# Optimization experiments

Hardware: AMD Instinct MI355X
Metric: run time of the kernel (lower is better)

The kernel has to match this reference:

```python
import jax, jax.numpy as jnp
import numpy as np

B = 16384; HB = 120; BD = 9; NS = 32; NF = 15  # history_bars, bar_descr, n_skills, n_forecast


def _lin_attn(x, wq, wk, wv, wo, bo, g, b):
    # x: [N, S, D_in]; linear attention with phi = elu + 1, residual + LayerNorm
    phi = lambda z: jax.nn.elu(z) + 1.0
    Q = phi(jnp.einsum('nsd,ed->nse', x, wq))
    K = phi(jnp.einsum('nsd,ed->nse', x, wk))
    V = jnp.einsum('nsd,ed->nse', x, wv)
    kv = jnp.einsum('nsd,nse->nde', K, V)              # [N, D, D]
    num = jnp.einsum('nsd,nde->nse', Q, kv)
    den = jnp.maximum(jnp.sum(Q * jnp.sum(K, axis=1, keepdims=True), axis=-1, keepdims=True), 1e-6)
    o = num / den
    y = jnp.einsum('nse,fe->nsf', o, wo) + bo + o      # out_proj + residual
    mu = jnp.mean(y, axis=-1, keepdims=True)
    var = jnp.var(y, axis=-1, keepdims=True)
    return (y - mu) * jax.lax.rsqrt(var + 1e-5) * g + b


def _forward(x, bn_g, bn_b, bn_m, bn_v, wq2, wk2, wv2, wo2, bo2, ln2g, ln2b,
             wq4, wk4, wv4, wo4, bo4, ln4g, ln4b,
             w_ih, w_hh, b_ih, b_hh, cg_w, cg_uw, cg_ub,
             w6, b6, w7, b7, rev_w, rev_b):
    Bn = x.shape[0]
    # BatchNorm1d (eval mode, running stats)
    out = (x - bn_m) * jax.lax.rsqrt(bn_v + 1e-5) * bn_g + bn_b
    # lin_attn_2: tokens = 120 time steps, d = 9 variables
    out = _lin_attn(out.reshape(Bn, HB, BD), wq2, wk2, wv2, wo2, bo2, ln2g, ln2b)
    # transpose_3: [B, 120, 9] -> [B, 9, 120]
    out = jnp.transpose(out, (0, 2, 1))
    # lin_attn_4: 9 parallel sequences of one 120-dim token
    out = _lin_attn(out.reshape(Bn * BD, 1, HB), wq4, wk4, wv4, wo4, bo4, ln4g, ln4b)
    # CGLSTM over 120 steps, vectorized across (batch * 9 variables)
    xs = jnp.transpose(out.reshape(Bn * BD, HB, 1), (1, 0, 2))  # [120, B*9, 1]
    h0 = jnp.zeros((Bn * BD, NS), x.dtype)

    def step(carry, x_t):
        h, c = carry
        gates = x_t @ w_ih.T + b_ih + h @ w_hh.T + b_hh  # [N, 4*NS]
        i, f, g, o = jnp.split(gates, 4, axis=-1)         # torch LSTMCell gate order
        c_new = jax.nn.sigmoid(f) * c + jax.nn.sigmoid(i) * jnp.tanh(g)
        gc = jax.nn.sigmoid(x_t @ cg_w.T + h @ cg_uw.T + cg_ub)  # contextual gate uses old h
        h_new = gc * jnp.tanh(c_new)                      # LSTM's own h output is discarded
        return (h_new, c_new), None

    (h, _), _ = jax.lax.scan(step, (h0, h0), xs)
    cglstm_out = h.reshape(Bn, BD * NS)                   # [B, 288]
    # conv_6 (pointwise per variable) + softplus, conv_7 + tanh
    t = jax.nn.softplus(h @ w6.T + b6)                    # [B*9, 60]
    t = jnp.tanh(t @ w7.T + b7).reshape(Bn, NF * BD)      # [B, 135]
    # transpose_8: view [B,15,9] -> [B,9,15]
    y = jnp.transpose(t.reshape(Bn, NF, BD), (0, 2, 1)).reshape(Bn, -1)
    # RevIN (normalize over full 135-dim vector, unbiased std as in torch.std)
    mu = jnp.mean(y, axis=-1, keepdims=True)
    sd = jnp.maximum(jnp.std(y, axis=-1, keepdims=True, ddof=1), 1e-5)
    enc = (y - mu) / sd * rev_w + rev_b
    return cglstm_out, enc


def setup_inputs() -> dict:
    key = jax.random.key(0)
    ks = jax.random.split(key, 20)
    r = lambda i, s, sc=0.1: jax.random.normal(ks[i], s, jnp.float32) * sc
    return dict(
        x=jax.random.normal(ks[0], (B, HB * BD), jnp.float32),
        bn_g=jnp.ones((HB * BD,), jnp.float32), bn_b=jnp.zeros((HB * BD,), jnp.float32),
        bn_m=r(1, (HB * BD,)),
        bn_v=jax.random.uniform(ks[2], (HB * BD,), jnp.float32, 0.5, 1.5),
        wq2=r(3, (BD, BD), 0.3), wk2=r(4, (BD, BD), 0.3), wv2=r(5, (BD, BD), 0.3),
        wo2=r(6, (BD, BD), 0.3), bo2=jnp.zeros((BD,), jnp.float32),
        ln2g=jnp.ones((BD,), jnp.float32), ln2b=jnp.zeros((BD,), jnp.float32),
        wq4=r(7, (HB, HB), 0.05), wk4=r(8, (HB, HB), 0.05), wv4=r(9, (HB, HB), 0.05),
        wo4=r(10, (HB, HB), 0.05), bo4=jnp.zeros((HB,), jnp.float32),
        ln4g=jnp.ones((HB,), jnp.float32), ln4b=jnp.zeros((HB,), jnp.float32),
        w_ih=r(11, (4 * NS, 1), 0.2), w_hh=r(12, (4 * NS, NS), 0.1),
        b_ih=jnp.zeros((4 * NS,), jnp.float32), b_hh=jnp.zeros((4 * NS,), jnp.float32),
        cg_w=r(13, (NS, 1), 0.2), cg_uw=r(14, (NS, NS), 0.1), cg_ub=jnp.zeros((NS,), jnp.float32),
        w6=r(15, (4 * NF, NS), 0.15), b6=jnp.zeros((4 * NF,), jnp.float32),
        w7=r(16, (NF, 4 * NF), 0.15), b7=jnp.zeros((NF,), jnp.float32),
        rev_w=jnp.ones((BD * NF,), jnp.float32), rev_b=jnp.zeros((BD * NF,), jnp.float32),
    )


def reference(x, bn_g, bn_b, bn_m, bn_v, wq2, wk2, wv2, wo2, bo2, ln2g, ln2b,
              wq4, wk4, wv4, wo4, bo4, ln4g, ln4b,
              w_ih, w_hh, b_ih, b_hh, cg_w, cg_uw, cg_ub,
              w6, b6, w7, b7, rev_w, rev_b):
    return _forward(x, bn_g, bn_b, bn_m, bn_v, wq2, wk2, wv2, wo2, bo2, ln2g, ln2b,
                    wq4, wk4, wv4, wo4, bo4, ln4g, ln4b,
                    w_ih, w_hh, b_ih, b_hh, cg_w, cg_uw, cg_ub,
                    w6, b6, w7, b7, rev_w, rev_b)
```

## Files before the change

kernel.cpp:

```cpp
#include <hip/hip_runtime.h>
#include <math.h>

#define NTH 256
#define SB 7

typedef __attribute__((ext_vector_type(8))) short bf16x8;
typedef __attribute__((ext_vector_type(4))) float f32x4;

__device__ __forceinline__ float fast_sigmoid(float x) {
    return __builtin_amdgcn_rcpf(1.0f + __expf(-x));
}
__device__ __forceinline__ float fast_tanh(float x) {
    return fmaf(-2.0f, __builtin_amdgcn_rcpf(__expf(2.0f * x) + 1.0f), 1.0f);
}
__device__ __forceinline__ short f2bf(float x) {
    unsigned u = __float_as_uint(x);
    return (short)((u + 0x7FFFu + ((u >> 16) & 1u)) >> 16);
}

extern "C" __global__ void __launch_bounds__(NTH, 3)
se_kernel(const float* __restrict__ x,
          const float* __restrict__ bn_g, const float* __restrict__ bn_b,
          const float* __restrict__ bn_m, const float* __restrict__ bn_v,
          const float* __restrict__ wq2, const float* __restrict__ wk2,
          const float* __restrict__ wv2, const float* __restrict__ wo2,
          const float* __restrict__ bo2, const float* __restrict__ ln2g,
          const float* __restrict__ ln2b,
          const float* __restrict__ wq4, const float* __restrict__ wk4,
          const float* __restrict__ wv4, const float* __restrict__ wo4,
          const float* __restrict__ bo4, const float* __restrict__ ln4g,
          const float* __restrict__ ln4b,
          const float* __restrict__ w_ih, const float* __restrict__ w_hh,
          const float* __restrict__ b_ih, const float* __restrict__ b_hh,
          const float* __restrict__ cg_w, const float* __restrict__ cg_uw,
          const float* __restrict__ cg_ub,
          const float* __restrict__ w6, const float* __restrict__ b6,
          const float* __restrict__ w7, const float* __restrict__ b7,
          const float* __restrict__ rev_w, const float* __restrict__ rev_b,
          float* __restrict__ out, int Bn)
{
    __shared__ __align__(16) float sm[13552];
    const int tid  = threadIdx.x;
    const int lane = tid & 63;
    const int wv   = tid >> 6;
    const int b0   = blockIdx.x * SB;
    const int nsamp = min(SB, Bn - b0);

    float* sU  = sm;
    float* SCR = sm + 7560;
    float* sWQ2 = sm + 13192; float* sWK2 = sm + 13273;
    float* sWV2 = sm + 13354; float* sWO2 = sm + 13435;
    float* sBO2 = sm + 13516; float* sLN2G = sm + 13525; float* sLN2B = sm + 13534;
    float* sKV = sm + 11880;  float* sKS = sm + 11961;
    float* sBO4 = sm + 13192; float* sLN4G = sm + 13312; float* sLN4B = sm + 13432;
    float* sMU = sm + 11880;  float* sRS = sm + 11900;
    float* sST = sm + 11920;
    float* sH0 = SCR;
    float* sH1 = SCR + 2816;
    float* sT1 = sU;
    float* sTF = sU + 3780;

    for (int i = tid; i < 81; i += NTH) {
        sWQ2[i] = wq2[i]; sWK2[i] = wk2[i]; sWV2[i] = wv2[i]; sWO2[i] = wo2[i];
    }
    if (tid < 9) { sBO2[tid] = bo2[tid]; sLN2G[tid] = ln2g[tid]; sLN2B[tid] = ln2b[tid]; }
    __syncthreads();

    float* S0 = SCR; float* S1 = SCR + 1080; float* S2 = SCR + 2160; float* S3 = SCR + 3240;
    for (int ss = 0; ss < SB; ++ss) {
        if (ss < nsamp) {
            const int b = b0 + ss;
            for (int i = tid; i < 1080; i += NTH) {
                float xv = x[(size_t)b * 1080 + i];
                S0[i] = (xv - bn_m[i]) * rsqrtf(bn_v[i] + 1e-5f) * bn_g[i] + bn_b[i];
            }
            __syncthreads();
            for (int idx = tid; idx < 1080; idx += NTH) {
                int s = idx / 9, e = idx - s * 9;
                float aq = 0.f, ak = 0.f, av = 0.f;
                #pragma unroll
                for (int d = 0; d < 9; ++d) {
                    float xv = S0[s * 9 + d];
                    aq = fmaf(xv, sWQ2[e * 9 + d], aq);
                    ak = fmaf(xv, sWK2[e * 9 + d], ak);
                    av = fmaf(xv, sWV2[e * 9 + d], av);
                }
                S1[idx] = aq >= 0.f ? aq + 1.f : __expf(aq);
                S2[idx] = ak >= 0.f ? ak + 1.f : __expf(ak);
                S3[idx] = av;
            }
            __syncthreads();
            if (tid < 81) {
                int d = tid / 9, e = tid - d * 9;
                float acc = 0.f;
                for (int s = 0; s < 120; ++s) acc = fmaf(S2[s * 9 + d], S3[s * 9 + e], acc);
                sKV[tid] = acc;
            } else if (tid < 90) {
                int d = tid - 81;
                float acc = 0.f;
                for (int s = 0; s < 120; ++s) acc += S2[s * 9 + d];
                sKS[d] = acc;
            }
            __syncthreads();
            for (int idx = tid; idx < 1080; idx += NTH) {
                int s = idx / 9, e = idx - s * 9;
                float num = 0.f, den = 0.f;
                #pragma unroll
                for (int d = 0; d < 9; ++d) {
                    float qv = S1[s * 9 + d];
                    num = fmaf(qv, sKV[d * 9 + e], num);
                    den = fmaf(qv, sKS[d], den);
                }
                S0[idx] = num / fmaxf(den, 1e-6f);
            }
            __syncthreads();
            for (int idx = tid; idx < 1080; idx += NTH) {
                int s = idx / 9, f = idx - s * 9;
                float acc = sBO2[f] + S0[s * 9 + f];
                #pragma unroll
                for (int e = 0; e < 9; ++e) acc = fmaf(S0[s * 9 + e], sWO2[f * 9 + e], acc);
                S1[idx] = acc;
            }
            __syncthreads();
            if (tid < 120) {
                int s = tid;
                float sum = 0.f, sq = 0.f;
                #pragma unroll
                for (int f = 0; f < 9; ++f) { float v = S1[s * 9 + f]; sum += v; sq = fmaf(v, v, sq); }
                float mu = sum * (1.f / 9.f);
                float rs = rsqrtf(sq * (1.f / 9.f) - mu * mu + 1e-5f);
                #pragma unroll
                for (int f = 0; f < 9; ++f)
                    sU[(ss * 9 + f) * 120 + s] = (S1[s * 9 + f] - mu) * rs * sLN2G[f] + sLN2B[f];
            }
        }
        __syncthreads();
    }

    for (int i = tid; i < 120; i += NTH) { sBO4[i] = bo4[i]; sLN4G[i] = ln4g[i]; sLN4B[i] = ln4b[i]; }
    for (int p = 0; p < 4; ++p) {
        float* V0 = SCR;
        float* Y0 = SCR + 2160;
        const int sp = tid / 120, erow = tid - sp * 120;
        const int smp = p * 2 + sp;
        const bool act = (tid < 240) && (smp < SB);
        if (act) {
            const float* uB = sU + smp * 1080;
            float acc[9];
            #pragma unroll
            for (int v = 0; v < 9; ++v) acc[v] = 0.f;
            const float* w0p = &wv4[erow * 120];
            for (int dq = 0; dq < 30; ++dq) {
                float4 wA = *(const float4*)&w0p[dq * 4];
                #pragma unroll
                for (int v = 0; v < 9; ++v) {
                    float4 u = *(const float4*)&uB[v * 120 + dq * 4];
                    acc[v] = fmaf(wA.x, u.x, acc[v]); acc[v] = fmaf(wA.y, u.y, acc[v]);
                    acc[v] = fmaf(wA.z, u.z, acc[v]); acc[v] = fmaf(wA.w, u.w, acc[v]);
                }
            }
            float* dst = V0 + sp * 1080;
            #pragma unroll
            for (int v = 0; v < 9; ++v) dst[v * 120 + erow] = acc[v];
        }
        __syncthreads();
        if (act) {
            const float* vB = V0 + sp * 1080;
            float acc[9];
            #pragma unroll
            for (int v = 0; v < 9; ++v) acc[v] = 0.f;
            const float* w0p = &wo4[erow * 120];
            for (int dq = 0; dq < 30; ++dq) {
                float4 wA = *(const float4*)&w0p[dq * 4];
                #pragma unroll
                for (int v = 0; v < 9; ++v) {
                    float4 u = *(const float4*)&vB[v * 120 + dq * 4];
                    acc[v] = fmaf(wA.x, u.x, acc[v]); acc[v] = fmaf(wA.y, u.y, acc[v]);
                    acc[v] = fmaf(wA.z, u.z, acc[v]); acc[v] = fmaf(wA.w, u.w, acc[v]);
                }
            }
            float* Y = Y0 + sp * 1080;
            #pragma unroll
            for (int v = 0; v < 9; ++v)
                Y[v * 120 + erow] = acc[v] + sBO4[erow] + vB[v * 120 + erow];
        }
        __syncthreads();
        if (tid < 18 && (p * 2 + tid / 9) < SB) {
            int sp2 = tid / 9, v = tid - sp2 * 9;
            const float* Y = Y0 + sp2 * 1080 + v * 120;
            float sum = 0.f, sq = 0.f;
            for (int e = 0; e < 120; ++e) { float t = Y[e]; sum += t; sq = fmaf(t, t, sq); }
            float mu = sum * (1.f / 120.f);
            sMU[tid] = mu;
            sRS[tid] = rsqrtf(sq * (1.f / 120.f) - mu * mu + 1e-5f);
        }
        __syncthreads();
        for (int idx = tid; idx < 540; idx += NTH) {
            int sp2 = idx / 270, off = idx - sp2 * 270;
            int smp2 = p * 2 + sp2;
            int v = off / 30, qq = off - v * 30;
            if (smp2 < SB) {
                const float* Y = Y0 + sp2 * 1080;
                float4 y = *(const float4*)&Y[v * 120 + qq * 4];
                float4 g = *(const float4*)&sLN4G[qq * 4];
                float4 bb = *(const float4*)&sLN4B[qq * 4];
                float mu = sMU[sp2 * 9 + v], rs = sRS[sp2 * 9 + v];
                float4 o;
                o.x = (y.x - mu) * rs * g.x + bb.x;
                o.y = (y.y - mu) * rs * g.y + bb.y;
                o.z = (y.z - mu) * rs * g.z + bb.z;
                o.w = (y.w - mu) * rs * g.w + bb.w;
                *(float4*)&sU[(smp2 * 9 + v) * 120 + qq * 4] = o;
            }
        }
        __syncthreads();
    }

    for (int i = tid; i < 2816; i += NTH) sH0[i] = 0.f;
    __syncthreads();

    const int c = lane & 15, q = lane >> 4;
    bf16x8 bfr[8]; float wxv[8], bsv[8];
    int grow[4]; int pcol;
    {
        bf16x8 pa, pb, pa2, pb2;
        #pragma unroll
        for (int j = 0; j < 8; ++j) { pa[j] = 0; pb[j] = 0; pa2[j] = 0; pb2[j] = 0; }
        if (q == 0) {
            pa[0]  = f2bf((float)c); pb[0]  = f2bf(1.0f);
            pa2[0] = f2bf(1.0f);     pb2[0] = f2bf((float)c);
        }
        f32x4 zc; zc[0] = zc[1] = zc[2] = zc[3] = 0.f;
        f32x4 prr = __builtin_amdgcn_mfma_f32_16x16x32_bf16(pa,  pb,  zc, 0, 0, 0);
        f32x4 pcc = __builtin_amdgcn_mfma_f32_16x16x32_bf16(pa2, pb2, zc, 0, 0, 0);
        #pragma unroll
        for (int r = 0; r < 4; ++r) grow[r] = wv * 16 + (int)(prr[r] + 0.5f);
        pcol = (int)(pcc[0] + 0.5f);

        #pragma unroll
        for (int T = 0; T < 8; ++T) {
            int gate = T >> 1, kk = ((T & 1) << 4) + pcol;
            const float* wr; float wx, bs;
            if (gate < 3) {
                int n = gate * 32 + kk;
                wr = &w_hh[n * 32]; wx = w_ih[n]; bs = b_ih[n] + b_hh[n];
            } else {
                wr = &cg_uw[kk * 32]; wx = cg_w[kk]; bs = cg_ub[kk];
            }
            bf16x8 tv;
            #pragma unroll
            for (int j = 0; j < 8; ++j) tv[j] = f2bf(wr[q * 8 + j]);
            bfr[T] = tv; wxv[T] = wx; bsv[T] = bs;
        }
    }
    float cst[8];
    #pragma unroll
    for (int i = 0; i < 8; ++i) cst[i] = 0.f;
    const int live9 = nsamp * 9;
    const float* ar0 = &sH0[(wv * 16 + c) * 44 + q * 8];
    const float* ar1 = &sH1[(wv * 16 + c) * 44 + q * 8];

#define LSTM_STEP(RP, WPL, XARR)                                               \
    {                                                                          \
        float4 hA = *(const float4*)(RP);                                      \
        float4 hB = *(const float4*)((RP) + 4);                                \
        bf16x8 af;                                                             \
        af[0] = f2bf(hA.x); af[1] = f2bf(hA.y);                                \
        af[2] = f2bf(hA.z); af[3] = f2bf(hA.w);                                \
        af[4] = f2bf(hB.x); af[5] = f2bf(hB.y);                                \
        af[6] = f2bf(hB.z); af[7] = f2bf(hB.w);                                \
        f32x4 acc[8];                                                          \
        _Pragma("unroll")                                                      \
        for (int T = 0; T < 8; ++T) {                                          \
            f32x4 ci;                                                          \
            _Pragma("unroll")                                                  \
            for (int r = 0; r < 4; ++r) ci[r] = fmaf(wxv[T], XARR[r], bsv[T]); \
            acc[T] = __builtin_amdgcn_mfma_f32_16x16x32_bf16(af, bfr[T], ci, 0, 0, 0); \
        }                                                                      \
        _Pragma("unroll")                                                      \
        for (int kh = 0; kh < 2; ++kh) {                                       \
            _Pragma("unroll")                                                  \
            for (int r = 0; r < 4; ++r) {                                      \
                float si  = fast_sigmoid(acc[kh][r]);                          \
                float sf  = fast_sigmoid(acc[2 + kh][r]);                      \
                float tg  = fast_tanh(acc[4 + kh][r]);                         \
                float sgc = fast_sigmoid(acc[6 + kh][r]);                      \
                float cn = fmaf(sf, cst[kh * 4 + r], si * tg);                 \
                cst[kh * 4 + r] = cn;                                          \
                (WPL)[grow[r] * 44 + (kh << 4) + pcol] = sgc * fast_tanh(cn);  \
            }                                                                  \
        }                                                                      \
    }

    for (int t = 0; t < 120; t += 2) {
        float xa[4], xb[4];
        #pragma unroll
        for (int r = 0; r < 4; ++r) {
            float2 xv;
            if (grow[r] < live9) xv = *(const float2*)&sU[grow[r] * 120 + t];
            else { xv.x = 0.f; xv.y = 0.f; }
            xa[r] = xv.x; xb[r] = xv.y;
        }
        LSTM_STEP(ar0, sH1, xa)
        LSTM_STEP(ar1, sH0, xb)
    }
    __syncthreads();

    for (int idx = tid; idx < SB * 288; idx += NTH) {
        int ssd = idx / 288, r = idx - ssd * 288;
        if (ssd < nsamp) {
            int v = r >> 5, k = r & 31;
            out[(size_t)(b0 + ssd) * 288 + r] = sH0[(ssd * 9 + v) * 44 + k];
        }
    }

    for (int idx = tid; idx < SB * 540; idx += NTH) {
        int ssd = idx / 540, rem = idx - ssd * 540;
        int v = rem / 60, j = rem - v * 60;
        if (ssd < nsamp) {
            float acc = b6[j];
            const float4* wr4 = (const float4*)&w6[j * 32];
            const float4* hv = (const float4*)&sH0[(ssd * 9 + v) * 44];
            #pragma unroll
            for (int qq = 0; qq < 8; ++qq) {
                float4 w = wr4[qq], h = hv[qq];
                acc = fmaf(w.x, h.x, acc); acc = fmaf(w.y, h.y, acc);
                acc = fmaf(w.z, h.z, acc); acc = fmaf(w.w, h.w, acc);
            }
            sT1[idx] = acc > 15.f ? acc : log1pf(__expf(acc));
        }
    }
    __syncthreads();
    for (int idx = tid; idx < SB * 135; idx += NTH) {
        int ssd = idx / 135, rem = idx - ssd * 135;
        int v = rem / 15, f = rem - v * 15;
        if (ssd < nsamp) {
            float acc = b7[f];
            const float4* wr = (const float4*)&w7[f * 60];
            const float4* tv = (const float4*)&sT1[ssd * 540 + v * 60];
            #pragma unroll
            for (int qq = 0; qq < 15; ++qq) {
                float4 w = wr[qq], h = tv[qq];
                acc = fmaf(w.x, h.x, acc); acc = fmaf(w.y, h.y, acc);
                acc = fmaf(w.z, h.z, acc); acc = fmaf(w.w, h.w, acc);
            }
            sTF[idx] = fast_tanh(acc);
        }
    }
    __syncthreads();
    if (tid < SB && tid < nsamp) {
        const float* tf = &sTF[tid * 135];
        float sum = 0.f;
        for (int i = 0; i < 135; ++i) sum += tf[i];
        float mu = sum * (1.f / 135.f);
        float sq = 0.f;
        for (int i = 0; i < 135; ++i) { float d = tf[i] - mu; sq = fmaf(d, d, sq); }
        float sd = sqrtf(sq * (1.f / 134.f));
        sST[tid * 2]     = mu;
        sST[tid * 2 + 1] = 1.f / fmaxf(sd, 1e-5f);
    }
    __syncthreads();
    const size_t encbase = (size_t)Bn * 288;
    for (int idx = tid; idx < SB * 135; idx += NTH) {
        int ssd = idx / 135, j = idx - ssd * 135;
        if (ssd < nsamp) {
            int qq = j / 15, pp = j - qq * 15;
            float val = (sTF[ssd * 135 + pp * 9 + qq] - sST[ssd * 2]) * sST[ssd * 2 + 1] * rev_w[j] + rev_b[j];
            out[encbase + (size_t)(b0 + ssd) * 135 + j] = val;
        }
    }
}

extern "C" void kernel_launch(void* const* d_in, const int* in_sizes, int n_in,
                              void* d_out, int out_size, void* d_ws, size_t ws_size,
                              hipStream_t stream) {
    const float* x    = (const float*)d_in[0];
    const float* bn_g = (const float*)d_in[1];
    const float* bn_b = (const float*)d_in[2];
    const float* bn_m = (const float*)d_in[3];
    const float* bn_v = (const float*)d_in[4];
    const float* wq2  = (const float*)d_in[5];
    const float* wk2  = (const float*)d_in[6];
    const float* wv2  = (const float*)d_in[7];
    const float* wo2  = (const float*)d_in[8];
    const float* bo2  = (const float*)d_in[9];
    const float* ln2g = (const float*)d_in[10];
    const float* ln2b = (const float*)d_in[11];
    const float* wq4  = (const float*)d_in[12];
    const float* wk4  = (const float*)d_in[13];
    const float* wv4  = (const float*)d_in[14];
    const float* wo4  = (const float*)d_in[15];
    const float* bo4  = (const float*)d_in[16];
    const float* ln4g = (const float*)d_in[17];
    const float* ln4b = (const float*)d_in[18];
    const float* w_ih = (const float*)d_in[19];
    const float* w_hh = (const float*)d_in[20];
    const float* b_ih = (const float*)d_in[21];
    const float* b_hh = (const float*)d_in[22];
    const float* cg_w = (const float*)d_in[23];
    const float* cg_uw= (const float*)d_in[24];
    const float* cg_ub= (const float*)d_in[25];
    const float* w6   = (const float*)d_in[26];
    const float* b6   = (const float*)d_in[27];
    const float* w7   = (const float*)d_in[28];
    const float* b7   = (const float*)d_in[29];
    const float* rev_w= (const float*)d_in[30];
    const float* rev_b= (const float*)d_in[31];

    int Bn = in_sizes[0] / 1080;
    int grid = (Bn + SB - 1) / SB;
    hipLaunchKernelGGL(se_kernel, dim3(grid), dim3(NTH), 0, stream,
                       x, bn_g, bn_b, bn_m, bn_v, wq2, wk2, wv2, wo2, bo2, ln2g, ln2b,
                       wq4, wk4, wv4, wo4, bo4, ln4g, ln4b,
                       w_ih, w_hh, b_ih, b_hh, cg_w, cg_uw, cg_ub,
                       w6, b6, w7, b7, rev_w, rev_b,
                       (float*)d_out, Bn);
}
```

Baseline: 1.524 ms.

## Store intermediate activations in bf16 shared memory and use packed bf16 conversion

Stores the per-sample activation buffer sU as bf16 instead of fp32. This halves its shared-memory footprint and shrinks the LDS allocation from about 54KB to about 39KB, so more blocks may fit per CU. It also swaps the manual float-to-bf16 rounding in the LSTM step for the hardware v_cvt_pk_bf16_f32 instruction. The cost is lower precision for inputs to the attention projection and the LSTM, plus extra unpack shifts on every read.

```diff
diff --git a/kernel.cpp b/kernel.cpp
--- a/kernel.cpp
+++ b/kernel.cpp
@@ -6,6 +6,8 @@
 
 typedef __attribute__((ext_vector_type(8))) short bf16x8;
 typedef __attribute__((ext_vector_type(4))) float f32x4;
+typedef __attribute__((ext_vector_type(2))) unsigned short us2;
+typedef __attribute__((ext_vector_type(4))) unsigned short us4;
 
 __device__ __forceinline__ float fast_sigmoid(float x) {
     return __builtin_amdgcn_rcpf(1.0f + __expf(-x));
@@ -16,6 +18,14 @@
 __device__ __forceinline__ short f2bf(float x) {
     unsigned u = __float_as_uint(x);
     return (short)((u + 0x7FFFu + ((u >> 16) & 1u)) >> 16);
+}
+__device__ __forceinline__ unsigned pk_bf16(float lo, float hi) {
+    unsigned r;
+    asm("v_cvt_pk_bf16_f32 %0, %1, %2" : "=v"(r) : "v"(lo), "v"(hi));
+    return r;
+}
+__device__ __forceinline__ float bf2f(unsigned short u) {
+    return __uint_as_float(((unsigned)u) << 16);
 }
 
 extern "C" __global__ void __launch_bounds__(NTH, 3)
@@ -39,26 +49,26 @@
           const float* __restrict__ rev_w, const float* __restrict__ rev_b,
           float* __restrict__ out, int Bn)
 {
-    __shared__ __align__(16) float sm[13552];
+    __shared__ __align__(16) float sm[9862];
     const int tid  = threadIdx.x;
     const int lane = tid & 63;
     const int wv   = tid >> 6;
     const int b0   = blockIdx.x * SB;
     const int nsamp = min(SB, Bn - b0);
 
-    float* sU  = sm;
-    float* SCR = sm + 7560;
-    float* sWQ2 = sm + 13192; float* sWK2 = sm + 13273;
-    float* sWV2 = sm + 13354; float* sWO2 = sm + 13435;
-    float* sBO2 = sm + 13516; float* sLN2G = sm + 13525; float* sLN2B = sm + 13534;
-    float* sKV = sm + 11880;  float* sKS = sm + 11961;
-    float* sBO4 = sm + 13192; float* sLN4G = sm + 13312; float* sLN4B = sm + 13432;
-    float* sMU = sm + 11880;  float* sRS = sm + 11900;
-    float* sST = sm + 11920;
+    unsigned short* sUb = (unsigned short*)sm;
+    float* SCR = sm + 3780;
+    float* sKV = sm + 9412; float* sKS = sm + 9493;
+    float* sMU = sm + 9412; float* sRS = sm + 9430;
+    float* sST = sm + 9448;
+    float* sWQ2 = sm + 9502; float* sWK2 = sm + 9583;
+    float* sWV2 = sm + 9664; float* sWO2 = sm + 9745;
+    float* sBO2 = sm + 9826; float* sLN2G = sm + 9835; float* sLN2B = sm + 9844;
+    float* sBO4 = sm + 9502; float* sLN4G = sm + 9622; float* sLN4B = sm + 9742;
     float* sH0 = SCR;
     float* sH1 = SCR + 2816;
-    float* sT1 = sU;
-    float* sTF = sU + 3780;
+    float* sT1 = sm;
+    float* sTF = SCR + 2816;
 
     for (int i = tid; i < 81; i += NTH) {
         sWQ2[i] = wq2[i]; sWK2[i] = wk2[i]; sWV2[i] = wv2[i]; sWO2[i] = wo2[i];
@@ -130,8 +140,10 @@
                 float mu = sum * (1.f / 9.f);
                 float rs = rsqrtf(sq * (1.f / 9.f) - mu * mu + 1e-5f);
                 #pragma unroll
-                for (int f = 0; f < 9; ++f)
-                    sU[(ss * 9 + f) * 120 + s] = (S1[s * 9 + f] - mu) * rs * sLN2G[f] + sLN2B[f];
+                for (int f = 0; f < 9; ++f) {
+                    float uo = (S1[s * 9 + f] - mu) * rs * sLN2G[f] + sLN2B[f];
+                    sUb[(ss * 9 + f) * 120 + s] = (unsigned short)f2bf(uo);
+                }
             }
         }
         __syncthreads();
@@ -145,7 +157,7 @@
         const int smp = p * 2 + sp;
         const bool act = (tid < 240) && (smp < SB);
         if (act) {
-            const float* uB = sU + smp * 1080;
+            const unsigned short* uBb = sUb + smp * 1080;
             float acc[9];
             #pragma unroll
             for (int v = 0; v < 9; ++v) acc[v] = 0.f;
@@ -154,9 +166,11 @@
                 float4 wA = *(const float4*)&w0p[dq * 4];
                 #pragma unroll
                 for (int v = 0; v < 9; ++v) {
-                    float4 u = *(const float4*)&uB[v * 120 + dq * 4];
-                    acc[v] = fmaf(wA.x, u.x, acc[v]); acc[v] = fmaf(wA.y, u.y, acc[v]);
-                    acc[v] = fmaf(wA.z, u.z, acc[v]); acc[v] = fmaf(wA.w, u.w, acc[v]);
+                    us4 ub = *(const us4*)&uBb[v * 120 + dq * 4];
+                    float u0 = bf2f(ub[0]), u1 = bf2f(ub[1]);
+                    float u2 = bf2f(ub[2]), u3 = bf2f(ub[3]);
+                    acc[v] = fmaf(wA.x, u0, acc[v]); acc[v] = fmaf(wA.y, u1, acc[v]);
+                    acc[v] = fmaf(wA.z, u2, acc[v]); acc[v] = fmaf(wA.w, u3, acc[v]);
                 }
             }
             float* dst = V0 + sp * 1080;
@@ -205,12 +219,13 @@
                 float4 g = *(const float4*)&sLN4G[qq * 4];
                 float4 bb = *(const float4*)&sLN4B[qq * 4];
                 float mu = sMU[sp2 * 9 + v], rs = sRS[sp2 * 9 + v];
-                float4 o;
-                o.x = (y.x - mu) * rs * g.x + bb.x;
-                o.y = (y.y - mu) * rs * g.y + bb.y;
-                o.z = (y.z - mu) * rs * g.z + bb.z;
-                o.w = (y.w - mu) * rs * g.w + bb.w;
-                *(float4*)&sU[(smp2 * 9 + v) * 120 + qq * 4] = o;
+                float ox = (y.x - mu) * rs * g.x + bb.x;
+                float oy = (y.y - mu) * rs * g.y + bb.y;
+                float oz = (y.z - mu) * rs * g.z + bb.z;
+                float ow = (y.w - mu) * rs * g.w + bb.w;
+                unsigned w0 = pk_bf16(ox, oy), w1 = pk_bf16(oz, ow);
+                uint2 pk; pk.x = w0; pk.y = w1;
+                *(uint2*)&sUb[(smp2 * 9 + v) * 120 + qq * 4] = pk;
             }
         }
         __syncthreads();
@@ -264,18 +279,18 @@
     {                                                                          \
         float4 hA = *(const float4*)(RP);                                      \
         float4 hB = *(const float4*)((RP) + 4);                                \
-        bf16x8 af;                                                             \
-        af[0] = f2bf(hA.x); af[1] = f2bf(hA.y);                                \
-        af[2] = f2bf(hA.z); af[3] = f2bf(hA.w);                                \
-        af[4] = f2bf(hB.x); af[5] = f2bf(hB.y);                                \
-        af[6] = f2bf(hB.z); af[7] = f2bf(hB.w);                                \
+        union { unsigned u[4]; bf16x8 v; } afu;                                \
+        afu.u[0] = pk_bf16(hA.x, hA.y);                                        \
+        afu.u[1] = pk_bf16(hA.z, hA.w);                                        \
+        afu.u[2] = pk_bf16(hB.x, hB.y);                                        \
+        afu.u[3] = pk_bf16(hB.z, hB.w);                                        \
         f32x4 acc[8];                                                          \
         _Pragma("unroll")                                                      \
         for (int T = 0; T < 8; ++T) {                                          \
             f32x4 ci;                                                          \
             _Pragma("unroll")                                                  \
             for (int r = 0; r < 4; ++r) ci[r] = fmaf(wxv[T], XARR[r], bsv[T]); \
-            acc[T] = __builtin_amdgcn_mfma_f32_16x16x32_bf16(af, bfr[T], ci, 0, 0, 0); \
+            acc[T] = __builtin_amdgcn_mfma_f32_16x16x32_bf16(afu.v, bfr[T], ci, 0, 0, 0); \
         }                                                                      \
         _Pragma("unroll")                                                      \
         for (int kh = 0; kh < 2; ++kh) {                                       \
@@ -296,10 +311,10 @@
         float xa[4], xb[4];
         #pragma unroll
         for (int r = 0; r < 4; ++r) {
-            float2 xv;
-            if (grow[r] < live9) xv = *(const float2*)&sU[grow[r] * 120 + t];
-            else { xv.x = 0.f; xv.y = 0.f; }
-            xa[r] = xv.x; xb[r] = xv.y;
+            if (grow[r] < live9) {
+                us2 xv = *(const us2*)&sUb[grow[r] * 120 + t];
+                xa[r] = bf2f(xv[0]); xb[r] = bf2f(xv[1]);
+            } else { xa[r] = 0.f; xb[r] = 0.f; }
         }
         LSTM_STEP(ar0, sH1, xa)
         LSTM_STEP(ar1, sH0, xb)
```

After: 1.321 ms. -13.3%, faster.
